# Optimization experiments

Hardware: AMD Instinct MI355X
Metric: run time of the kernel (lower is better)

Reference implementation:

```python
import jax, jax.numpy as jnp
import numpy as np

T = 8192
H = 512
OUT = 2


def _lstm_layer(x, h0, c0, W_ih, W_hh, b_ih, b_hh):
    """Unidirectional LSTM layer, PyTorch gate order (i, f, g, o).
    x: (T, H_in); h0, c0: (H,). Returns (T, H) hidden sequence."""
    b = b_ih + b_hh  # (4H,)
    # Precompute input projections for all timesteps in one GEMM: (T, 4H)
    xg = x @ W_ih.T + b

    def step(carry, xgt):
        h, c = carry
        g = xgt + h @ W_hh.T  # (4H,)
        i, f, gg, o = jnp.split(g, 4)
        i = jax.nn.sigmoid(i)
        f = jax.nn.sigmoid(f)
        gg = jnp.tanh(gg)
        o = jax.nn.sigmoid(o)
        c = f * c + i * gg
        h = o * jnp.tanh(c)
        return (h, c), h

    (_, _), hs = jax.lax.scan(step, (h0, c0), xg)
    return hs


def setup_inputs() -> dict:
    key = jax.random.key(0)
    ks = jax.random.split(key, 16)
    bound = 1.0 / np.sqrt(H)

    def u(k, shape):
        return jax.random.uniform(k, shape, jnp.float32, -bound, bound)

    inp = {
        "tensor_data": jax.random.normal(ks[0], (T, 1, H), jnp.float32),
        "truth_v": jax.random.uniform(ks[1], (T, 1, OUT), jnp.float32),
        "h0": jax.random.normal(ks[2], (2, 1, H), jnp.float32),
        "c0": jax.random.normal(ks[3], (2, 1, H), jnp.float32),
        # layer 0 LSTM params (PyTorch layout: weight_ih (4H, H_in))
        "W_ih0": u(ks[4], (4 * H, H)),
        "W_hh0": u(ks[5], (4 * H, H)),
        "b_ih0": u(ks[6], (4 * H,)),
        "b_hh0": u(ks[7], (4 * H,)),
        # layer 1 LSTM params
        "W_ih1": u(ks[8], (4 * H, H)),
        "W_hh1": u(ks[9], (4 * H, H)),
        "b_ih1": u(ks[10], (4 * H,)),
        "b_hh1": u(ks[11], (4 * H,)),
        # linear head
        "W_head": u(ks[12], (OUT, H)),
        "b_head": u(ks[13], (OUT,)),
    }
    return inp


def reference(tensor_data, truth_v, h0, c0,
              W_ih0, W_hh0, b_ih0, b_hh0,
              W_ih1, W_hh1, b_ih1, b_hh1,
              W_head, b_head):
    x = tensor_data[:, 0, :]  # (T, H), batch = 1
    h1 = _lstm_layer(x, h0[0, 0], c0[0, 0], W_ih0, W_hh0, b_ih0, b_hh0)
    h2 = _lstm_layer(h1, h0[1, 0], c0[1, 0], W_ih1, W_hh1, b_ih1, b_hh1)
    logits = h2 @ W_head.T + b_head  # (T, OUT)
    p = jax.nn.sigmoid(logits)
    y = truth_v[:, 0, :]
    # BCELoss (mean reduction); clamp logs at -100 like torch.nn.BCELoss
    log_p = jnp.maximum(jnp.log(p), -100.0)
    log_1mp = jnp.maximum(jnp.log1p(-p), -100.0)
    loss = -jnp.mean(y * log_p + (1.0 - y) * log_1mp)
    return loss
```

## Files before the change

kernel.cpp:

```cpp
#include <hip/hip_runtime.h>
#include <stdint.h>

#define TSTEPS 8192
#define HDIM 512
#define G4 2048

typedef unsigned long long ull;

__device__ __forceinline__ ull pack_th(unsigned tag, float v) {
    union { float f; unsigned u; } x; x.f = v;
    return ((ull)tag << 32) | (ull)x.u;
}
__device__ __forceinline__ float unpack_v(ull p) {
    union { unsigned u; float f; } x; x.u = (unsigned)p;
    return x.f;
}

__global__ __launch_bounds__(256, 1) void lstm_fused(
    const float* __restrict__ x,
    const float* __restrict__ Whh0,
    const float* __restrict__ Wih0,
    const float* __restrict__ bih0,
    const float* __restrict__ bhh0,
    const float* __restrict__ Wih1,
    const float* __restrict__ Whh1,
    const float* __restrict__ bih1,
    const float* __restrict__ bhh1,
    const float* __restrict__ h0,
    const float* __restrict__ c0,
    float* __restrict__ h2seq,
    ull* __restrict__ ring0,
    ull* __restrict__ ring1)
{
    const int L2   = (blockIdx.x >= 64) ? 1 : 0;
    const int w    = L2 ? (int)blockIdx.x - 64 : (int)blockIdx.x;
    const int tid  = threadIdx.x;
    const int wave = tid >> 6;
    const int lane = tid & 63;
    const int jj   = lane >> 5;
    const int g    = (lane >> 3) & 3;
    const int kk   = lane & 7;
    const int j    = w * 8 + wave * 2 + jj;
    const int row  = g * HDIM + j;

    float4 wqA[16], wqB[16];
    {
        const float* WA = L2 ? Whh1 : Whh0;
        const float* WB = L2 ? Wih1 : Wih0;
        const float4* wpA = (const float4*)(WA + (size_t)row * HDIM + kk * 64);
        const float4* wpB = (const float4*)(WB + (size_t)row * HDIM + kk * 64);
#pragma unroll
        for (int u = 0; u < 16; ++u) wqA[u] = wpA[(u + kk) & 15];
#pragma unroll
        for (int u = 0; u < 16; ++u) wqB[u] = wpB[(u + kk) & 15];
    }
    const float bias = L2 ? (bih1[row] + bhh1[row]) : (bih0[row] + bhh0[row]);
    float c = c0[(L2 ? HDIM : 0) + j];

    const bool pub = (lane == jj * 32);
    if (pub) {
        const float h = h0[(L2 ? HDIM : 0) + j];
        ull* r = L2 ? ring1 : ring0;
        __hip_atomic_store(&r[j], pack_th(1u, h),
                           __ATOMIC_RELAXED, __HIP_MEMORY_SCOPE_AGENT);
    }

    __shared__ float hA[HDIM];
    __shared__ float hB[HDIM];

    if (!L2) {
        float2 v = *(const float2*)&x[2 * tid];
        hB[2 * tid] = v.x; hB[2 * tid + 1] = v.y;
    } else {
        ull* s = ring0 + (size_t)1 * HDIM;
        ull p0 = __hip_atomic_load(&s[2 * tid],     __ATOMIC_RELAXED, __HIP_MEMORY_SCOPE_AGENT);
        ull p1 = __hip_atomic_load(&s[2 * tid + 1], __ATOMIC_RELAXED, __HIP_MEMORY_SCOPE_AGENT);
        while ((unsigned)(p0 >> 32) != 2u || (unsigned)(p1 >> 32) != 2u) {
            __builtin_amdgcn_s_sleep(1);
            p0 = __hip_atomic_load(&s[2 * tid],     __ATOMIC_RELAXED, __HIP_MEMORY_SCOPE_AGENT);
            p1 = __hip_atomic_load(&s[2 * tid + 1], __ATOMIC_RELAXED, __HIP_MEMORY_SCOPE_AGENT);
        }
        hB[2 * tid]     = unpack_v(p0);
        hB[2 * tid + 1] = unpack_v(p1);
    }
    __syncthreads();

    for (int t = 0; t < TSTEPS; ++t) {
        float2 xnext;
        if (!L2) {
            const int rn = (t + 1 < TSTEPS) ? t + 1 : 0;
            xnext = *(const float2*)&x[(size_t)rn * HDIM + 2 * tid];
        }
        float p0f = 0.f, p1f = 0.f, p2f = 0.f, p3f = 0.f;
        {
            const float4* hb4 = (const float4*)&hB[kk * 64];
#pragma unroll
            for (int u = 0; u < 16; ++u) {
                const float4 hv = hb4[(u + kk) & 15];
                p0f += wqB[u].x * hv.x; p1f += wqB[u].y * hv.y;
                p2f += wqB[u].z * hv.z; p3f += wqB[u].w * hv.w;
            }
        }
        const float pre = (p0f + p1f) + (p2f + p3f);

        {
            ull* s = L2 ? (ring1 + (size_t)(t & 1) * HDIM)
                        : (ring0 + (size_t)t * HDIM);
            const unsigned tg = (unsigned)(t + 1);
            ull q0 = __hip_atomic_load(&s[2 * tid],     __ATOMIC_RELAXED, __HIP_MEMORY_SCOPE_AGENT);
            ull q1 = __hip_atomic_load(&s[2 * tid + 1], __ATOMIC_RELAXED, __HIP_MEMORY_SCOPE_AGENT);
            while ((unsigned)(q0 >> 32) != tg || (unsigned)(q1 >> 32) != tg) {
                __builtin_amdgcn_s_sleep(1);
                q0 = __hip_atomic_load(&s[2 * tid],     __ATOMIC_RELAXED, __HIP_MEMORY_SCOPE_AGENT);
                q1 = __hip_atomic_load(&s[2 * tid + 1], __ATOMIC_RELAXED, __HIP_MEMORY_SCOPE_AGENT);
            }
            hA[2 * tid]     = unpack_v(q0);
            hA[2 * tid + 1] = unpack_v(q1);
        }
        __syncthreads();

        float s0 = 0.f, s1 = 0.f, s2 = 0.f, s3 = 0.f;
        {
            const float4* ha4 = (const float4*)&hA[kk * 64];
#pragma unroll
            for (int u = 0; u < 16; ++u) {
                const float4 hv = ha4[(u + kk) & 15];
                s0 += wqA[u].x * hv.x; s1 += wqA[u].y * hv.y;
                s2 += wqA[u].z * hv.z; s3 += wqA[u].w * hv.w;
            }
        }
        float s = (s0 + s1) + (s2 + s3) + pre;

        s += __shfl_xor(s, 1);
        s += __shfl_xor(s, 2);
        s += __shfl_xor(s, 4);
        s += bias;

        const float sc  = (g == 2) ? 2.f : 1.f;
        const float sig = 1.f / (1.f + __expf(-sc * s));
        const float act = sc * sig - (sc - 1.f);

        const int base = jj * 32 + kk;
        const float iv = __shfl(act, base);
        const float fv = __shfl(act, base + 8);
        const float gv = __shfl(act, base + 16);
        const float ov = __shfl(act, base + 24);

        c = fv * c + iv * gv;
        const float h = ov * (1.f - 2.f / (__expf(2.f * c) + 1.f));

        if (pub) {
            if (!L2) {
                __hip_atomic_store(&ring0[(size_t)(t + 1) * HDIM + j],
                                   pack_th((unsigned)(t + 2), h),
                                   __ATOMIC_RELAXED, __HIP_MEMORY_SCOPE_AGENT);
            } else {
                __hip_atomic_store(&ring1[(size_t)((t + 1) & 1) * HDIM + j],
                                   pack_th((unsigned)(t + 2), h),
                                   __ATOMIC_RELAXED, __HIP_MEMORY_SCOPE_AGENT);
            }
        }
        if (L2 && lane == jj * 32 + 1)
            h2seq[(size_t)t * HDIM + j] = h;

        if (t + 1 < TSTEPS) {
            if (!L2) {
                hB[2 * tid] = xnext.x; hB[2 * tid + 1] = xnext.y;
            } else {
                ull* s2p = ring0 + (size_t)(t + 2) * HDIM;
                const unsigned tg2 = (unsigned)(t + 3);
                ull q0 = __hip_atomic_load(&s2p[2 * tid],     __ATOMIC_RELAXED, __HIP_MEMORY_SCOPE_AGENT);
                ull q1 = __hip_atomic_load(&s2p[2 * tid + 1], __ATOMIC_RELAXED, __HIP_MEMORY_SCOPE_AGENT);
                while ((unsigned)(q0 >> 32) != tg2 || (unsigned)(q1 >> 32) != tg2) {
                    __builtin_amdgcn_s_sleep(1);
                    q0 = __hip_atomic_load(&s2p[2 * tid],     __ATOMIC_RELAXED, __HIP_MEMORY_SCOPE_AGENT);
                    q1 = __hip_atomic_load(&s2p[2 * tid + 1], __ATOMIC_RELAXED, __HIP_MEMORY_SCOPE_AGENT);
                }
                hB[2 * tid]     = unpack_v(q0);
                hB[2 * tid + 1] = unpack_v(q1);
            }
            __syncthreads();
        }
    }
}

__global__ __launch_bounds__(256) void head_loss(
    const float* __restrict__ h2,
    const float* __restrict__ Wh,
    const float* __restrict__ bh,
    const float* __restrict__ y,
    float* __restrict__ out)
{
    const int tid  = threadIdx.x;
    const int lane = tid & 63;
    const int wv   = tid >> 6;
    const int gw   = blockIdx.x * 4 + wv;

    float w0[8], w1[8];
#pragma unroll
    for (int u = 0; u < 8; ++u) {
        w0[u] = Wh[lane * 8 + u];
        w1[u] = Wh[HDIM + lane * 8 + u];
    }

    float lsum = 0.f;
    for (int t = gw; t < TSTEPS; t += 1024) {
        const float* hp = h2 + (size_t)t * HDIM + lane * 8;
        float4 hv0 = *(const float4*)&hp[0];
        float4 hv1 = *(const float4*)&hp[4];
        float a0 = hv0.x * w0[0] + hv0.y * w0[1] + hv0.z * w0[2] + hv0.w * w0[3]
                 + hv1.x * w0[4] + hv1.y * w0[5] + hv1.z * w0[6] + hv1.w * w0[7];
        float a1 = hv0.x * w1[0] + hv0.y * w1[1] + hv0.z * w1[2] + hv0.w * w1[3]
                 + hv1.x * w1[4] + hv1.y * w1[5] + hv1.z * w1[6] + hv1.w * w1[7];
#pragma unroll
        for (int m = 1; m < 64; m <<= 1) {
            a0 += __shfl_xor(a0, m);
            a1 += __shfl_xor(a1, m);
        }
        if (lane == 0) {
            const float z0 = a0 + bh[0];
            const float z1 = a1 + bh[1];
            const float p0 = 1.f / (1.f + __expf(-z0));
            const float p1 = 1.f / (1.f + __expf(-z1));
            const float lp0  = fmaxf(__logf(p0), -100.f);
            const float lp1  = fmaxf(__logf(p1), -100.f);
            const float l1p0 = fmaxf(log1pf(-p0), -100.f);
            const float l1p1 = fmaxf(log1pf(-p1), -100.f);
            const float y0 = y[(size_t)t * 2 + 0];
            const float y1 = y[(size_t)t * 2 + 1];
            lsum += y0 * lp0 + (1.f - y0) * l1p0;
            lsum += y1 * lp1 + (1.f - y1) * l1p1;
        }
    }

    __shared__ float red[4];
    if (lane == 0) red[wv] = lsum;
    __syncthreads();
    if (tid == 0) {
        const float ssum = red[0] + red[1] + red[2] + red[3];
        atomicAdd(out, ssum * (-1.f / (float)(TSTEPS * 2)));
    }
}

extern "C" void kernel_launch(void* const* d_in, const int* in_sizes, int n_in,
                              void* d_out, int out_size, void* d_ws, size_t ws_size,
                              hipStream_t stream)
{
    const float* x     = (const float*)d_in[0];
    const float* truth = (const float*)d_in[1];
    const float* h0    = (const float*)d_in[2];
    const float* c0    = (const float*)d_in[3];
    const float* Wih0  = (const float*)d_in[4];
    const float* Whh0  = (const float*)d_in[5];
    const float* bih0  = (const float*)d_in[6];
    const float* bhh0  = (const float*)d_in[7];
    const float* Wih1  = (const float*)d_in[8];
    const float* Whh1  = (const float*)d_in[9];
    const float* bih1  = (const float*)d_in[10];
    const float* bhh1  = (const float*)d_in[11];
    const float* Whead = (const float*)d_in[12];
    const float* bhead = (const float*)d_in[13];

    char* ws = (char*)d_ws;
    ull*   ring0 = (ull*)ws;
    ull*   ring1 = (ull*)(ws + (((size_t)34) << 20));
    float* h2seq = (float*)(ws + (((size_t)35) << 20));

    hipMemsetAsync(d_out, 0, (size_t)out_size * sizeof(float), stream);

    lstm_fused<<<128, 256, 0, stream>>>(x, Whh0, Wih0, bih0, bhh0,
                                        Wih1, Whh1, bih1, bhh1,
                                        h0, c0, h2seq, ring0, ring1);
    head_loss<<<256, 256, 0, stream>>>(h2seq, Whead, bhead, truth, (float*)d_out);
}
```

Baseline: 14.80 ms.

## Give each wave one hidden unit and poll ring buffers directly without LDS barriers

Work is remapped so each wave owns a single hidden unit across all four gates. The grid doubles to 256 blocks and each lane keeps 8 weights per gate in registers. Each wave now reads h straight from the global ring buffer into registers, spinning first on a sentinel element and then on its own 8 slots. This removes the shared-memory staging and all __syncthreads from the step loop. Layer 1's ring is no longer double-buffered; it becomes a full-length sequence, with the workspace offsets moved to match. The cost is a full 64-lane butterfly reduction per gate and 8 times more global polling traffic per block.

```diff
diff --git a/kernel.cpp b/kernel.cpp
--- a/kernel.cpp
+++ b/kernel.cpp
@@ -3,7 +3,6 @@
 
 #define TSTEPS 8192
 #define HDIM 512
-#define G4 2048
 
 typedef unsigned long long ull;
 
@@ -32,154 +31,165 @@
     ull* __restrict__ ring0,
     ull* __restrict__ ring1)
 {
-    const int L2   = (blockIdx.x >= 64) ? 1 : 0;
-    const int w    = L2 ? (int)blockIdx.x - 64 : (int)blockIdx.x;
+    const int L2   = (blockIdx.x >= 128) ? 1 : 0;
+    const int wb   = L2 ? (int)blockIdx.x - 128 : (int)blockIdx.x;
     const int tid  = threadIdx.x;
     const int wave = tid >> 6;
     const int lane = tid & 63;
-    const int jj   = lane >> 5;
-    const int g    = (lane >> 3) & 3;
-    const int kk   = lane & 7;
-    const int j    = w * 8 + wave * 2 + jj;
-    const int row  = g * HDIM + j;
-
-    float4 wqA[16], wqB[16];
+    const int j    = wb * 4 + wave;
+    const int SENT = (j + 257) & 511;
+
+    float wA[4][8], wB[4][8];
     {
         const float* WA = L2 ? Whh1 : Whh0;
         const float* WB = L2 ? Wih1 : Wih0;
-        const float4* wpA = (const float4*)(WA + (size_t)row * HDIM + kk * 64);
-        const float4* wpB = (const float4*)(WB + (size_t)row * HDIM + kk * 64);
-#pragma unroll
-        for (int u = 0; u < 16; ++u) wqA[u] = wpA[(u + kk) & 15];
-#pragma unroll
-        for (int u = 0; u < 16; ++u) wqB[u] = wpB[(u + kk) & 15];
-    }
-    const float bias = L2 ? (bih1[row] + bhh1[row]) : (bih0[row] + bhh0[row]);
+#pragma unroll
+        for (int r = 0; r < 4; ++r) {
+            const size_t rb = (size_t)(r * HDIM + j) * HDIM + lane;
+#pragma unroll
+            for (int u = 0; u < 8; ++u) {
+                wA[r][u] = WA[rb + 64 * u];
+                wB[r][u] = WB[rb + 64 * u];
+            }
+        }
+    }
+    float bb[4];
+#pragma unroll
+    for (int r = 0; r < 4; ++r)
+        bb[r] = L2 ? (bih1[r * HDIM + j] + bhh1[r * HDIM + j])
+                   : (bih0[r * HDIM + j] + bhh0[r * HDIM + j]);
     float c = c0[(L2 ? HDIM : 0) + j];
 
-    const bool pub = (lane == jj * 32);
-    if (pub) {
-        const float h = h0[(L2 ? HDIM : 0) + j];
-        ull* r = L2 ? ring1 : ring0;
-        __hip_atomic_store(&r[j], pack_th(1u, h),
+    ull* rring = L2 ? ring1 : ring0;
+
+    if (lane == 0)
+        __hip_atomic_store(&rring[j], pack_th(1u, h0[(L2 ? HDIM : 0) + j]),
                            __ATOMIC_RELAXED, __HIP_MEMORY_SCOPE_AGENT);
-    }
-
-    __shared__ float hA[HDIM];
-    __shared__ float hB[HDIM];
-
+
+    float fv[8];
     if (!L2) {
-        float2 v = *(const float2*)&x[2 * tid];
-        hB[2 * tid] = v.x; hB[2 * tid + 1] = v.y;
+#pragma unroll
+        for (int u = 0; u < 8; ++u) fv[u] = x[lane + 64 * u];
     } else {
-        ull* s = ring0 + (size_t)1 * HDIM;
-        ull p0 = __hip_atomic_load(&s[2 * tid],     __ATOMIC_RELAXED, __HIP_MEMORY_SCOPE_AGENT);
-        ull p1 = __hip_atomic_load(&s[2 * tid + 1], __ATOMIC_RELAXED, __HIP_MEMORY_SCOPE_AGENT);
-        while ((unsigned)(p0 >> 32) != 2u || (unsigned)(p1 >> 32) != 2u) {
-            __builtin_amdgcn_s_sleep(1);
-            p0 = __hip_atomic_load(&s[2 * tid],     __ATOMIC_RELAXED, __HIP_MEMORY_SCOPE_AGENT);
-            p1 = __hip_atomic_load(&s[2 * tid + 1], __ATOMIC_RELAXED, __HIP_MEMORY_SCOPE_AGENT);
-        }
-        hB[2 * tid]     = unpack_v(p0);
-        hB[2 * tid + 1] = unpack_v(p1);
-    }
-    __syncthreads();
+        {
+            const ull* sent = ring0 + (size_t)1 * HDIM + SENT;
+            while ((unsigned)(__hip_atomic_load(sent, __ATOMIC_RELAXED,
+                                                __HIP_MEMORY_SCOPE_AGENT) >> 32) != 2u)
+                __builtin_amdgcn_s_sleep(1);
+        }
+        const ull* s = ring0 + (size_t)1 * HDIM + lane;
+        ull p[8];
+#pragma unroll
+        for (int u = 0; u < 8; ++u)
+            p[u] = __hip_atomic_load(&s[64 * u], __ATOMIC_RELAXED, __HIP_MEMORY_SCOPE_AGENT);
+        bool ok;
+        do {
+            ok = true;
+#pragma unroll
+            for (int u = 0; u < 8; ++u)
+                if ((unsigned)(p[u] >> 32) != 2u) {
+                    p[u] = __hip_atomic_load(&s[64 * u], __ATOMIC_RELAXED, __HIP_MEMORY_SCOPE_AGENT);
+                    ok &= ((unsigned)(p[u] >> 32) == 2u);
+                }
+        } while (!ok);
+#pragma unroll
+        for (int u = 0; u < 8; ++u) fv[u] = unpack_v(p[u]);
+    }
 
     for (int t = 0; t < TSTEPS; ++t) {
-        float2 xnext;
-        if (!L2) {
-            const int rn = (t + 1 < TSTEPS) ? t + 1 : 0;
-            xnext = *(const float2*)&x[(size_t)rn * HDIM + 2 * tid];
-        }
-        float p0f = 0.f, p1f = 0.f, p2f = 0.f, p3f = 0.f;
+        float hv[8];
         {
-            const float4* hb4 = (const float4*)&hB[kk * 64];
-#pragma unroll
-            for (int u = 0; u < 16; ++u) {
-                const float4 hv = hb4[(u + kk) & 15];
-                p0f += wqB[u].x * hv.x; p1f += wqB[u].y * hv.y;
-                p2f += wqB[u].z * hv.z; p3f += wqB[u].w * hv.w;
+            const unsigned tg = (unsigned)(t + 1);
+            {
+                const ull* sent = rring + (size_t)t * HDIM + SENT;
+                while ((unsigned)(__hip_atomic_load(sent, __ATOMIC_RELAXED,
+                                                    __HIP_MEMORY_SCOPE_AGENT) >> 32) != tg)
+                    __builtin_amdgcn_s_sleep(1);
             }
-        }
-        const float pre = (p0f + p1f) + (p2f + p3f);
-
-        {
-            ull* s = L2 ? (ring1 + (size_t)(t & 1) * HDIM)
-                        : (ring0 + (size_t)t * HDIM);
-            const unsigned tg = (unsigned)(t + 1);
-            ull q0 = __hip_atomic_load(&s[2 * tid],     __ATOMIC_RELAXED, __HIP_MEMORY_SCOPE_AGENT);
-            ull q1 = __hip_atomic_load(&s[2 * tid + 1], __ATOMIC_RELAXED, __HIP_MEMORY_SCOPE_AGENT);
-            while ((unsigned)(q0 >> 32) != tg || (unsigned)(q1 >> 32) != tg) {
-                __builtin_amdgcn_s_sleep(1);
-                q0 = __hip_atomic_load(&s[2 * tid],     __ATOMIC_RELAXED, __HIP_MEMORY_SCOPE_AGENT);
-                q1 = __hip_atomic_load(&s[2 * tid + 1], __ATOMIC_RELAXED, __HIP_MEMORY_SCOPE_AGENT);
-            }
-            hA[2 * tid]     = unpack_v(q0);
-            hA[2 * tid + 1] = unpack_v(q1);
-        }
-        __syncthreads();
-
-        float s0 = 0.f, s1 = 0.f, s2 = 0.f, s3 = 0.f;
-        {
-            const float4* ha4 = (const float4*)&hA[kk * 64];
-#pragma unroll
-            for (int u = 0; u < 16; ++u) {
-                const float4 hv = ha4[(u + kk) & 15];
-                s0 += wqA[u].x * hv.x; s1 += wqA[u].y * hv.y;
-                s2 += wqA[u].z * hv.z; s3 += wqA[u].w * hv.w;
-            }
-        }
-        float s = (s0 + s1) + (s2 + s3) + pre;
-
-        s += __shfl_xor(s, 1);
-        s += __shfl_xor(s, 2);
-        s += __shfl_xor(s, 4);
-        s += bias;
-
-        const float sc  = (g == 2) ? 2.f : 1.f;
-        const float sig = 1.f / (1.f + __expf(-sc * s));
-        const float act = sc * sig - (sc - 1.f);
-
-        const int base = jj * 32 + kk;
-        const float iv = __shfl(act, base);
-        const float fv = __shfl(act, base + 8);
-        const float gv = __shfl(act, base + 16);
-        const float ov = __shfl(act, base + 24);
-
-        c = fv * c + iv * gv;
+            const ull* s = rring + (size_t)t * HDIM + lane;
+            ull p[8];
+#pragma unroll
+            for (int u = 0; u < 8; ++u)
+                p[u] = __hip_atomic_load(&s[64 * u], __ATOMIC_RELAXED, __HIP_MEMORY_SCOPE_AGENT);
+            bool ok;
+            do {
+                ok = true;
+#pragma unroll
+                for (int u = 0; u < 8; ++u)
+                    if ((unsigned)(p[u] >> 32) != tg) {
+                        p[u] = __hip_atomic_load(&s[64 * u], __ATOMIC_RELAXED, __HIP_MEMORY_SCOPE_AGENT);
+                        ok &= ((unsigned)(p[u] >> 32) == tg);
+                    }
+            } while (!ok);
+#pragma unroll
+            for (int u = 0; u < 8; ++u) hv[u] = unpack_v(p[u]);
+        }
+
+        float a0 = 0.f, a1 = 0.f, a2 = 0.f, a3 = 0.f;
+#pragma unroll
+        for (int u = 0; u < 8; ++u) {
+            a0 += wA[0][u] * hv[u]; a1 += wA[1][u] * hv[u];
+            a2 += wA[2][u] * hv[u]; a3 += wA[3][u] * hv[u];
+        }
+#pragma unroll
+        for (int u = 0; u < 8; ++u) {
+            a0 += wB[0][u] * fv[u]; a1 += wB[1][u] * fv[u];
+            a2 += wB[2][u] * fv[u]; a3 += wB[3][u] * fv[u];
+        }
+
+#pragma unroll
+        for (int m = 1; m < 64; m <<= 1) {
+            a0 += __shfl_xor(a0, m);
+            a1 += __shfl_xor(a1, m);
+            a2 += __shfl_xor(a2, m);
+            a3 += __shfl_xor(a3, m);
+        }
+
+        const float iv = 1.f / (1.f + __expf(-(a0 + bb[0])));
+        const float ff = 1.f / (1.f + __expf(-(a1 + bb[1])));
+        const float gg = 1.f - 2.f / (__expf(2.f * (a2 + bb[2])) + 1.f);
+        const float ov = 1.f / (1.f + __expf(-(a3 + bb[3])));
+        c = ff * c + iv * gg;
         const float h = ov * (1.f - 2.f / (__expf(2.f * c) + 1.f));
 
-        if (pub) {
-            if (!L2) {
-                __hip_atomic_store(&ring0[(size_t)(t + 1) * HDIM + j],
-                                   pack_th((unsigned)(t + 2), h),
-                                   __ATOMIC_RELAXED, __HIP_MEMORY_SCOPE_AGENT);
-            } else {
-                __hip_atomic_store(&ring1[(size_t)((t + 1) & 1) * HDIM + j],
-                                   pack_th((unsigned)(t + 2), h),
-                                   __ATOMIC_RELAXED, __HIP_MEMORY_SCOPE_AGENT);
-            }
-        }
-        if (L2 && lane == jj * 32 + 1)
+        if (lane == 0)
+            __hip_atomic_store(&rring[(size_t)(t + 1) * HDIM + j],
+                               pack_th((unsigned)(t + 2), h),
+                               __ATOMIC_RELAXED, __HIP_MEMORY_SCOPE_AGENT);
+        if (L2 && lane == 1)
             h2seq[(size_t)t * HDIM + j] = h;
 
         if (t + 1 < TSTEPS) {
             if (!L2) {
-                hB[2 * tid] = xnext.x; hB[2 * tid + 1] = xnext.y;
+#pragma unroll
+                for (int u = 0; u < 8; ++u)
+                    fv[u] = x[(size_t)(t + 1) * HDIM + lane + 64 * u];
             } else {
-                ull* s2p = ring0 + (size_t)(t + 2) * HDIM;
-                const unsigned tg2 = (unsigned)(t + 3);
-                ull q0 = __hip_atomic_load(&s2p[2 * tid],     __ATOMIC_RELAXED, __HIP_MEMORY_SCOPE_AGENT);
-                ull q1 = __hip_atomic_load(&s2p[2 * tid + 1], __ATOMIC_RELAXED, __HIP_MEMORY_SCOPE_AGENT);
-                while ((unsigned)(q0 >> 32) != tg2 || (unsigned)(q1 >> 32) != tg2) {
-                    __builtin_amdgcn_s_sleep(1);
-                    q0 = __hip_atomic_load(&s2p[2 * tid],     __ATOMIC_RELAXED, __HIP_MEMORY_SCOPE_AGENT);
-                    q1 = __hip_atomic_load(&s2p[2 * tid + 1], __ATOMIC_RELAXED, __HIP_MEMORY_SCOPE_AGENT);
+                const unsigned tg = (unsigned)(t + 3);
+                {
+                    const ull* sent = ring0 + (size_t)(t + 2) * HDIM + SENT;
+                    while ((unsigned)(__hip_atomic_load(sent, __ATOMIC_RELAXED,
+                                                        __HIP_MEMORY_SCOPE_AGENT) >> 32) != tg)
+                        __builtin_amdgcn_s_sleep(2);
                 }
-                hB[2 * tid]     = unpack_v(q0);
-                hB[2 * tid + 1] = unpack_v(q1);
+                const ull* s = ring0 + (size_t)(t + 2) * HDIM + lane;
+                ull p[8];
+#pragma unroll
+                for (int u = 0; u < 8; ++u)
+                    p[u] = __hip_atomic_load(&s[64 * u], __ATOMIC_RELAXED, __HIP_MEMORY_SCOPE_AGENT);
+                bool ok;
+                do {
+                    ok = true;
+#pragma unroll
+                    for (int u = 0; u < 8; ++u)
+                        if ((unsigned)(p[u] >> 32) != tg) {
+                            p[u] = __hip_atomic_load(&s[64 * u], __ATOMIC_RELAXED, __HIP_MEMORY_SCOPE_AGENT);
+                            ok &= ((unsigned)(p[u] >> 32) == tg);
+                        }
+                } while (!ok);
+#pragma unroll
+                for (int u = 0; u < 8; ++u) fv[u] = unpack_v(p[u]);
             }
-            __syncthreads();
         }
     }
 }
@@ -264,11 +274,11 @@
     char* ws = (char*)d_ws;
     ull*   ring0 = (ull*)ws;
     ull*   ring1 = (ull*)(ws + (((size_t)34) << 20));
-    float* h2seq = (float*)(ws + (((size_t)35) << 20));
+    float* h2seq = (float*)(ws + (((size_t)68) << 20));
 
     hipMemsetAsync(d_out, 0, (size_t)out_size * sizeof(float), stream);
 
-    lstm_fused<<<128, 256, 0, stream>>>(x, Whh0, Wih0, bih0, bhh0,
+    lstm_fused<<<256, 256, 0, stream>>>(x, Whh0, Wih0, bih0, bhh0,
                                         Wih1, Whh1, bih1, bhh1,
                                         h0, c0, h2seq, ring0, ring1);
     head_loss<<<256, 256, 0, stream>>>(h2seq, Whead, bhead, truth, (float*)d_out);
```

Result: slower. 30.71 ms (+107.6%).

## Move LSTM weights from registers to LDS and double-buffer hidden inputs

Applied to the files above, without the earlier changes.

Stores each block's W_hh and W_ih slices in 128KB of dynamic LDS instead of 128 float4 registers per thread. The h and x/h1 buffers become double-buffered by step parity, which removes the second __syncthreads per timestep. The ring1 buffer for layer 2 becomes a full-length array like ring0, with h2seq moved to a later workspace offset. The aim is to cut register pressure and barrier count, at the cost of an extra LDS read of the weights on every step.

```diff
diff --git a/kernel.cpp b/kernel.cpp
--- a/kernel.cpp
+++ b/kernel.cpp
@@ -3,7 +3,7 @@
 
 #define TSTEPS 8192
 #define HDIM 512
-#define G4 2048
+#define LDS_BYTES 139264
 
 typedef unsigned long long ull;
 
@@ -32,6 +32,12 @@
     ull* __restrict__ ring0,
     ull* __restrict__ ring1)
 {
+    extern __shared__ float lds[];
+    float* sWA = lds;
+    float* sWB = lds + 16384;
+    float* hAb = lds + 32768;
+    float* hBb = lds + 33792;
+
     const int L2   = (blockIdx.x >= 64) ? 1 : 0;
     const int w    = L2 ? (int)blockIdx.x - 64 : (int)blockIdx.x;
     const int tid  = threadIdx.x;
@@ -40,39 +46,38 @@
     const int jj   = lane >> 5;
     const int g    = (lane >> 3) & 3;
     const int kk   = lane & 7;
-    const int j    = w * 8 + wave * 2 + jj;
-    const int row  = g * HDIM + j;
-
-    float4 wqA[16], wqB[16];
+    const int ju   = wave * 2 + jj;
+    const int j    = w * 8 + ju;
+    const int row_local = g * 8 + ju;
+    const int grow = g * HDIM + j;
+
+    ull* rring = L2 ? ring1 : ring0;
+
+    if (lane == jj * 32)
+        __hip_atomic_store(&rring[j], pack_th(1u, h0[(L2 ? HDIM : 0) + j]),
+                           __ATOMIC_RELAXED, __HIP_MEMORY_SCOPE_AGENT);
+
     {
         const float* WA = L2 ? Whh1 : Whh0;
         const float* WB = L2 ? Wih1 : Wih0;
-        const float4* wpA = (const float4*)(WA + (size_t)row * HDIM + kk * 64);
-        const float4* wpB = (const float4*)(WB + (size_t)row * HDIM + kk * 64);
-#pragma unroll
-        for (int u = 0; u < 16; ++u) wqA[u] = wpA[(u + kk) & 15];
-#pragma unroll
-        for (int u = 0; u < 16; ++u) wqB[u] = wpB[(u + kk) & 15];
-    }
-    const float bias = L2 ? (bih1[row] + bhh1[row]) : (bih0[row] + bhh0[row]);
-    float c = c0[(L2 ? HDIM : 0) + j];
-
-    const bool pub = (lane == jj * 32);
-    if (pub) {
-        const float h = h0[(L2 ? HDIM : 0) + j];
-        ull* r = L2 ? ring1 : ring0;
-        __hip_atomic_store(&r[j], pack_th(1u, h),
-                           __ATOMIC_RELAXED, __HIP_MEMORY_SCOPE_AGENT);
-    }
-
-    __shared__ float hA[HDIM];
-    __shared__ float hB[HDIM];
+        const int r   = tid >> 3;
+        const int sub = tid & 7;
+        const int rg  = r >> 3;
+        const int rju = r & 7;
+        const size_t gr = (size_t)(rg * HDIM + w * 8 + rju) * HDIM + sub * 64;
+        float4* dA = (float4*)&sWA[r * 512 + sub * 64];
+        float4* dB = (float4*)&sWB[r * 512 + sub * 64];
+        const float4* sA = (const float4*)&WA[gr];
+        const float4* sB = (const float4*)&WB[gr];
+#pragma unroll
+        for (int q = 0; q < 16; ++q) { dA[q] = sA[q]; dB[q] = sB[q]; }
+    }
 
     if (!L2) {
         float2 v = *(const float2*)&x[2 * tid];
-        hB[2 * tid] = v.x; hB[2 * tid + 1] = v.y;
+        hBb[2 * tid] = v.x; hBb[2 * tid + 1] = v.y;
     } else {
-        ull* s = ring0 + (size_t)1 * HDIM;
+        const ull* s = ring0 + (size_t)1 * HDIM;
         ull p0 = __hip_atomic_load(&s[2 * tid],     __ATOMIC_RELAXED, __HIP_MEMORY_SCOPE_AGENT);
         ull p1 = __hip_atomic_load(&s[2 * tid + 1], __ATOMIC_RELAXED, __HIP_MEMORY_SCOPE_AGENT);
         while ((unsigned)(p0 >> 32) != 2u || (unsigned)(p1 >> 32) != 2u) {
@@ -80,56 +85,59 @@
             p0 = __hip_atomic_load(&s[2 * tid],     __ATOMIC_RELAXED, __HIP_MEMORY_SCOPE_AGENT);
             p1 = __hip_atomic_load(&s[2 * tid + 1], __ATOMIC_RELAXED, __HIP_MEMORY_SCOPE_AGENT);
         }
-        hB[2 * tid]     = unpack_v(p0);
-        hB[2 * tid + 1] = unpack_v(p1);
-    }
+        hBb[2 * tid]     = unpack_v(p0);
+        hBb[2 * tid + 1] = unpack_v(p1);
+    }
+
+    const float bias = L2 ? (bih1[grow] + bhh1[grow]) : (bih0[grow] + bhh0[grow]);
+    float c = c0[(L2 ? HDIM : 0) + j];
+
     __syncthreads();
 
     for (int t = 0; t < TSTEPS; ++t) {
-        float2 xnext;
-        if (!L2) {
-            const int rn = (t + 1 < TSTEPS) ? t + 1 : 0;
-            xnext = *(const float2*)&x[(size_t)rn * HDIM + 2 * tid];
-        }
-        float p0f = 0.f, p1f = 0.f, p2f = 0.f, p3f = 0.f;
+        const int p = t & 1;
+
+        float2 xn;
+        if (!L2 && t + 1 < TSTEPS)
+            xn = *(const float2*)&x[(size_t)(t + 1) * HDIM + 2 * tid];
+
         {
-            const float4* hb4 = (const float4*)&hB[kk * 64];
-#pragma unroll
-            for (int u = 0; u < 16; ++u) {
-                const float4 hv = hb4[(u + kk) & 15];
-                p0f += wqB[u].x * hv.x; p1f += wqB[u].y * hv.y;
-                p2f += wqB[u].z * hv.z; p3f += wqB[u].w * hv.w;
+            const ull* s = rring + (size_t)t * HDIM;
+            const unsigned tg = (unsigned)(t + 1);
+            ull p0 = __hip_atomic_load(&s[2 * tid],     __ATOMIC_RELAXED, __HIP_MEMORY_SCOPE_AGENT);
+            ull p1 = __hip_atomic_load(&s[2 * tid + 1], __ATOMIC_RELAXED, __HIP_MEMORY_SCOPE_AGENT);
+            while ((unsigned)(p0 >> 32) != tg || (unsigned)(p1 >> 32) != tg) {
+                __builtin_amdgcn_s_sleep(1);
+                p0 = __hip_atomic_load(&s[2 * tid],     __ATOMIC_RELAXED, __HIP_MEMORY_SCOPE_AGENT);
+                p1 = __hip_atomic_load(&s[2 * tid + 1], __ATOMIC_RELAXED, __HIP_MEMORY_SCOPE_AGENT);
             }
-        }
-        const float pre = (p0f + p1f) + (p2f + p3f);
-
-        {
-            ull* s = L2 ? (ring1 + (size_t)(t & 1) * HDIM)
-                        : (ring0 + (size_t)t * HDIM);
-            const unsigned tg = (unsigned)(t + 1);
-            ull q0 = __hip_atomic_load(&s[2 * tid],     __ATOMIC_RELAXED, __HIP_MEMORY_SCOPE_AGENT);
-            ull q1 = __hip_atomic_load(&s[2 * tid + 1], __ATOMIC_RELAXED, __HIP_MEMORY_SCOPE_AGENT);
-            while ((unsigned)(q0 >> 32) != tg || (unsigned)(q1 >> 32) != tg) {
-                __builtin_amdgcn_s_sleep(1);
-                q0 = __hip_atomic_load(&s[2 * tid],     __ATOMIC_RELAXED, __HIP_MEMORY_SCOPE_AGENT);
-                q1 = __hip_atomic_load(&s[2 * tid + 1], __ATOMIC_RELAXED, __HIP_MEMORY_SCOPE_AGENT);
-            }
-            hA[2 * tid]     = unpack_v(q0);
-            hA[2 * tid + 1] = unpack_v(q1);
+            hAb[p * 512 + 2 * tid]     = unpack_v(p0);
+            hAb[p * 512 + 2 * tid + 1] = unpack_v(p1);
         }
         __syncthreads();
 
+        const float* wa = &sWA[row_local * 512 + kk * 64];
+        const float* wb = &sWB[row_local * 512 + kk * 64];
+        const float* ha = &hAb[p * 512 + kk * 64];
+        const float* hb = &hBb[p * 512 + kk * 64];
         float s0 = 0.f, s1 = 0.f, s2 = 0.f, s3 = 0.f;
-        {
-            const float4* ha4 = (const float4*)&hA[kk * 64];
-#pragma unroll
-            for (int u = 0; u < 16; ++u) {
-                const float4 hv = ha4[(u + kk) & 15];
-                s0 += wqA[u].x * hv.x; s1 += wqA[u].y * hv.y;
-                s2 += wqA[u].z * hv.z; s3 += wqA[u].w * hv.w;
-            }
-        }
-        float s = (s0 + s1) + (s2 + s3) + pre;
+#pragma unroll
+        for (int u = 0; u < 16; ++u) {
+            const int q = ((u + kk) & 15) * 4;
+            const float4 wq = *(const float4*)&wa[q];
+            const float4 hq = *(const float4*)&ha[q];
+            s0 += wq.x * hq.x; s1 += wq.y * hq.y;
+            s2 += wq.z * hq.z; s3 += wq.w * hq.w;
+        }
+#pragma unroll
+        for (int u = 0; u < 16; ++u) {
+            const int q = ((u + kk) & 15) * 4;
+            const float4 wq = *(const float4*)&wb[q];
+            const float4 hq = *(const float4*)&hb[q];
+            s0 += wq.x * hq.x; s1 += wq.y * hq.y;
+            s2 += wq.z * hq.z; s3 += wq.w * hq.w;
+        }
+        float s = (s0 + s1) + (s2 + s3);
 
         s += __shfl_xor(s, 1);
         s += __shfl_xor(s, 2);
@@ -149,37 +157,30 @@
         c = fv * c + iv * gv;
         const float h = ov * (1.f - 2.f / (__expf(2.f * c) + 1.f));
 
-        if (pub) {
-            if (!L2) {
-                __hip_atomic_store(&ring0[(size_t)(t + 1) * HDIM + j],
-                                   pack_th((unsigned)(t + 2), h),
-                                   __ATOMIC_RELAXED, __HIP_MEMORY_SCOPE_AGENT);
-            } else {
-                __hip_atomic_store(&ring1[(size_t)((t + 1) & 1) * HDIM + j],
-                                   pack_th((unsigned)(t + 2), h),
-                                   __ATOMIC_RELAXED, __HIP_MEMORY_SCOPE_AGENT);
-            }
-        }
+        if (lane == jj * 32)
+            __hip_atomic_store(&rring[(size_t)(t + 1) * HDIM + j],
+                               pack_th((unsigned)(t + 2), h),
+                               __ATOMIC_RELAXED, __HIP_MEMORY_SCOPE_AGENT);
         if (L2 && lane == jj * 32 + 1)
             h2seq[(size_t)t * HDIM + j] = h;
 
         if (t + 1 < TSTEPS) {
             if (!L2) {
-                hB[2 * tid] = xnext.x; hB[2 * tid + 1] = xnext.y;
+                hBb[(1 - p) * 512 + 2 * tid]     = xn.x;
+                hBb[(1 - p) * 512 + 2 * tid + 1] = xn.y;
             } else {
-                ull* s2p = ring0 + (size_t)(t + 2) * HDIM;
-                const unsigned tg2 = (unsigned)(t + 3);
-                ull q0 = __hip_atomic_load(&s2p[2 * tid],     __ATOMIC_RELAXED, __HIP_MEMORY_SCOPE_AGENT);
-                ull q1 = __hip_atomic_load(&s2p[2 * tid + 1], __ATOMIC_RELAXED, __HIP_MEMORY_SCOPE_AGENT);
-                while ((unsigned)(q0 >> 32) != tg2 || (unsigned)(q1 >> 32) != tg2) {
+                const ull* s2 = ring0 + (size_t)(t + 2) * HDIM;
+                const unsigned tg = (unsigned)(t + 3);
+                ull q0 = __hip_atomic_load(&s2[2 * tid],     __ATOMIC_RELAXED, __HIP_MEMORY_SCOPE_AGENT);
+                ull q1 = __hip_atomic_load(&s2[2 * tid + 1], __ATOMIC_RELAXED, __HIP_MEMORY_SCOPE_AGENT);
+                while ((unsigned)(q0 >> 32) != tg || (unsigned)(q1 >> 32) != tg) {
                     __builtin_amdgcn_s_sleep(1);
-                    q0 = __hip_atomic_load(&s2p[2 * tid],     __ATOMIC_RELAXED, __HIP_MEMORY_SCOPE_AGENT);
-                    q1 = __hip_atomic_load(&s2p[2 * tid + 1], __ATOMIC_RELAXED, __HIP_MEMORY_SCOPE_AGENT);
+                    q0 = __hip_atomic_load(&s2[2 * tid],     __ATOMIC_RELAXED, __HIP_MEMORY_SCOPE_AGENT);
+                    q1 = __hip_atomic_load(&s2[2 * tid + 1], __ATOMIC_RELAXED, __HIP_MEMORY_SCOPE_AGENT);
                 }
-                hB[2 * tid]     = unpack_v(q0);
-                hB[2 * tid + 1] = unpack_v(q1);
+                hBb[(1 - p) * 512 + 2 * tid]     = unpack_v(q0);
+                hBb[(1 - p) * 512 + 2 * tid + 1] = unpack_v(q1);
             }
-            __syncthreads();
         }
     }
 }
@@ -264,12 +265,15 @@
     char* ws = (char*)d_ws;
     ull*   ring0 = (ull*)ws;
     ull*   ring1 = (ull*)(ws + (((size_t)34) << 20));
-    float* h2seq = (float*)(ws + (((size_t)35) << 20));
+    float* h2seq = (float*)(ws + (((size_t)68) << 20));
 
     hipMemsetAsync(d_out, 0, (size_t)out_size * sizeof(float), stream);
 
-    lstm_fused<<<128, 256, 0, stream>>>(x, Whh0, Wih0, bih0, bhh0,
-                                        Wih1, Whh1, bih1, bhh1,
-                                        h0, c0, h2seq, ring0, ring1);
+    hipFuncSetAttribute((const void*)lstm_fused,
+                        hipFuncAttributeMaxDynamicSharedMemorySize, LDS_BYTES);
+
+    lstm_fused<<<128, 256, LDS_BYTES, stream>>>(x, Whh0, Wih0, bih0, bhh0,
+                                                Wih1, Whh1, bih1, bhh1,
+                                                h0, c0, h2seq, ring0, ring1);
     head_loss<<<256, 256, 0, stream>>>(h2seq, Whead, bhead, truth, (float*)d_out);
 }
```

New measurement: 14.76 ms. No clear change (-0.3%).
